# Kernel tuning notes

Hardware: AMD Instinct MI355X
Metric: run time of the kernel (lower is better)

Reference implementation:

```python
import jax, jax.numpy as jnp
import numpy as np

MIMO_RANK = 4  # module constant; q/k are identical across rank and mimo_v=mimo_out=ones,
               # q_bias=k_bias=0, so the rank sum equals MIMO_RANK * single-rank output.


def _rotary(t, ang):
    # split-half rotary: t [..., d], ang [..., d//2]
    d2 = t.shape[-1] // 2
    t1, t2 = t[..., :d2], t[..., d2:]
    c, s = jnp.cos(ang), jnp.sin(ang)
    return jnp.concatenate([t1 * c - t2 * s, t1 * s + t2 * c], axis=-1)


def setup_inputs() -> dict:
    key = jax.random.key(0)
    ks = jax.random.split(key, 6)
    b, l, h, dv, g, dqk = 2, 4096, 32, 64, 1, 128
    x = jax.random.normal(ks[0], (b, l, h, dv), jnp.float32)
    # positive step sizes (discretization dt)
    dt = jax.random.uniform(ks[1], (b, l, h), jnp.float32) * 0.05 + 1e-3
    # negative decay rates so exp(A*dt) < 1
    A = -(jax.random.uniform(ks[2], (h,), jnp.float32) + 0.5)
    B_gate = jax.random.normal(ks[3], (b, l, g, dqk), jnp.float32)
    C_gate = jax.random.normal(ks[4], (b, l, g, dqk), jnp.float32)
    D = jax.random.normal(ks[5], (h,), jnp.float32)
    return {"x": x, "dt": dt, "A": A, "B_gate": B_gate, "C_gate": C_gate,
            "D": D, "chunk_size": 64}


def reference(x, dt, A, B_gate, C_gate, D, chunk_size):
    # Mamba3 MIMO chunked selective scan (SSD) with rotary QK decay.
    # Recurrence per (b, h):  H_t = exp(A_h*dt_t) * H_{t-1} + rot(k_t) (dt_t x_t)^T
    #                         y_t = rot(q_t)^T H_t * MIMO_RANK + D_h * x_t
    # where q=C_gate, k=B_gate (shared across heads, ngroups=1) and the rotary
    # angle is theta_t = cumsum(dt) (TILELANG_ROTARY_DIV=2 -> dqk//2 angles).
    b, l, h, dv = x.shape
    dqk = C_gate.shape[-1]
    c = chunk_size
    n = l // c

    ang = jnp.cumsum(dt, axis=1)[..., None]                     # [b,l,h,1]
    ang = jnp.broadcast_to(ang, (b, l, h, dqk // 2))
    q = jnp.broadcast_to(C_gate[:, :, 0, :][:, :, None, :], (b, l, h, dqk))
    k = jnp.broadcast_to(B_gate[:, :, 0, :][:, :, None, :], (b, l, h, dqk))
    rotq = _rotary(q, ang)                                      # [b,l,h,dqk]
    rotk = _rotary(k, ang)
    adt = A[None, None, :] * dt                                 # [b,l,h] log-decay

    chunk = lambda t: t.reshape(b, n, c, *t.shape[2:])
    rq, rk = chunk(rotq), chunk(rotk)                           # [b,n,c,h,dqk]
    u = chunk(dt[..., None] * x)                                # [b,n,c,h,dv]
    a = chunk(adt)                                              # [b,n,c,h]
    cum = jnp.cumsum(a, axis=2)                                 # within-chunk cum log-decay

    # ---- intra-chunk (quadratic within chunk) ----
    seg = cum[:, :, :, None, :] - cum[:, :, None, :, :]         # [b,n,t,s,h]
    mask = jnp.tril(jnp.ones((c, c), bool))
    L = jnp.where(mask[None, None, :, :, None], jnp.exp(seg), 0.0)
    S = jnp.einsum('bnthd,bnshd->bntsh', rq, rk)                # [b,n,t,s,h]
    y_intra = jnp.einsum('bntsh,bnshe->bnthe', S * L, u)        # [b,n,c,h,dv]

    # ---- inter-chunk state recurrence ----
    decay_to_end = jnp.exp(cum[:, :, -1:, :] - cum)             # [b,n,c,h]
    dH = jnp.einsum('bnshd,bnsh,bnshe->bnhde', rk, decay_to_end, u)  # [b,n,h,dqk,dv]
    cdecay = jnp.exp(cum[:, :, -1, :])                          # [b,n,h] full-chunk decay

    def step(H, inp):
        dc, dh = inp
        Hprev = H
        return dc[:, :, None, None] * H + dh, Hprev

    H0 = jnp.zeros((b, h, dqk, dv), x.dtype)
    _, Hprev = jax.lax.scan(step, H0,
                            (jnp.moveaxis(cdecay, 1, 0), jnp.moveaxis(dH, 1, 0)))
    Hprev = jnp.moveaxis(Hprev, 0, 1)                           # [b,n,h,dqk,dv]

    y_inter = jnp.einsum('bnthd,bnth,bnhde->bnthe', rq, jnp.exp(cum), Hprev)

    y = MIMO_RANK * (y_intra + y_inter).reshape(b, l, h, dv)
    return y + D[None, None, :, None] * x
```

## Files before the change

kernel.cpp:

```cpp
#include <hip/hip_runtime.h>
#include <hip/hip_bf16.h>

#define BB 2
#define LL 4096
#define HH 32
#define DV 64
#define DQK 128
#define CC 64
#define NN 64
#define MIMO_RANK 4.0f

typedef __attribute__((ext_vector_type(8))) short short8;
typedef __attribute__((ext_vector_type(4))) float f32x4;

__device__ __forceinline__ ushort f2bf(float f) {
    uint u = __float_as_uint(f);
    u += 0x7FFF + ((u >> 16) & 1);
    return (ushort)(u >> 16);
}
__device__ __forceinline__ float bfbits2f(uint lo16) {
    return __uint_as_float(lo16 << 16);
}
__device__ __forceinline__ uint pkbf2(float lo, float hi) {
    return (uint)f2bf(lo) | ((uint)f2bf(hi) << 16);
}
union U8 { uint u[4]; short8 s; };

__device__ __forceinline__ int rk_off(int s, int d) {
    return s * 128 + (((((d >> 3) & 15) ^ (s & 7)) << 3)) + (d & 7);
}
__device__ __forceinline__ int rkT_off(int d, int s) {
    return d * 64 + ((((s >> 3) ^ (d & 7)) & 7) << 3) + (s & 7);
}
__device__ __forceinline__ int uwT_off(int e, int s) {
    return e * 64 + ((((s >> 3) ^ (e & 7)) & 7) << 3) + (s & 7);
}
__device__ __forceinline__ int fSL(int t) {
    return (((t & 3) << 1) ^ ((t >> 2) & 7)) & 7;
}
__device__ __forceinline__ int SL_off(int t, int s) {
    return t * 64 + ((((s >> 3) ^ fSL(t)) & 7) << 3) + (s & 7);
}

__device__ __forceinline__ void make_rot_frags(const float* __restrict__ G,
                                               size_t gb, float cv, float sv,
                                               int kgrp, short8* fr) {
    #pragma unroll
    for (int kk = 0; kk < 4; ++kk) {
        int d0 = kk * 32 + kgrp;
        int dl = d0 & 63;
        bool low = d0 < 64;
        float4 a1 = *(const float4*)(G + gb + dl);
        float4 b1 = *(const float4*)(G + gb + dl + 4);
        float4 a2 = *(const float4*)(G + gb + dl + 64);
        float4 b2 = *(const float4*)(G + gb + dl + 68);
        float v0, v1, v2, v3, v4, v5, v6, v7;
        if (low) {
            v0 = a1.x * cv - a2.x * sv; v1 = a1.y * cv - a2.y * sv;
            v2 = a1.z * cv - a2.z * sv; v3 = a1.w * cv - a2.w * sv;
            v4 = b1.x * cv - b2.x * sv; v5 = b1.y * cv - b2.y * sv;
            v6 = b1.z * cv - b2.z * sv; v7 = b1.w * cv - b2.w * sv;
        } else {
            v0 = a1.x * sv + a2.x * cv; v1 = a1.y * sv + a2.y * cv;
            v2 = a1.z * sv + a2.z * cv; v3 = a1.w * sv + a2.w * cv;
            v4 = b1.x * sv + b2.x * cv; v5 = b1.y * sv + b2.y * cv;
            v6 = b1.z * sv + b2.z * cv; v7 = b1.w * sv + b2.w * cv;
        }
        U8 r;
        r.u[0] = pkbf2(v0, v1); r.u[1] = pkbf2(v2, v3);
        r.u[2] = pkbf2(v4, v5); r.u[3] = pkbf2(v6, v7);
        fr[kk] = r.s;
    }
}

__global__ __launch_bounds__(256) void k_scan_dt(const float* __restrict__ dt,
                                                 float* __restrict__ ang) {
    int bh = blockIdx.x;
    int b = bh / HH, h = bh % HH;
    int tid = threadIdx.x;
    const int PT = LL / 256;
    float v[PT];
    float s = 0.f;
    int tbase = tid * PT;
    for (int i = 0; i < PT; ++i) {
        v[i] = dt[(((size_t)b * LL + tbase + i) * HH) + h];
        s += v[i];
    }
    int lane = tid & 63, wv = tid >> 6;
    float ps = s;
    for (int off = 1; off < 64; off <<= 1) {
        float o = __shfl_up(ps, off, 64);
        if (lane >= off) ps += o;
    }
    __shared__ float wsum[4];
    if (lane == 63) wsum[wv] = ps;
    __syncthreads();
    float wadd = 0.f;
    for (int w = 0; w < wv; ++w) wadd += wsum[w];
    float run = wadd + ps - s;
    for (int i = 0; i < PT; ++i) {
        run += v[i];
        ang[(((size_t)b * LL + tbase + i) * HH) + h] = run;
    }
}

__global__ __launch_bounds__(256, 3) void k_intra(
    const float* __restrict__ x, const float* __restrict__ dt,
    const float* __restrict__ A, const float* __restrict__ Bg,
    const float* __restrict__ Cg, const float* __restrict__ ang,
    const float* __restrict__ Dd,
    float* __restrict__ out, ushort* __restrict__ dH,
    float* __restrict__ cdecay) {
    int n = blockIdx.x, h = blockIdx.y, b = blockIdx.z;
    int tid = threadIdx.x;
    int t0 = n * CC;

    __shared__ ushort rkS[CC * DQK];
    __shared__ ushort rkT[DQK * CC];
    __shared__ ushort uwT[DV * CC];
    __shared__ ushort SLs[CC * CC];
    __shared__ float angs[CC], csv[CC], ssv[CC], dw2[CC];

    float Ah = A[h];

    float my_dt = 0.f;
    if (tid < CC) {
        float a = ang[(((size_t)b * LL + t0 + tid) * HH) + h];
        angs[tid] = a;
        float sv, cv;
        __sincosf(a, &sv, &cv);
        csv[tid] = cv;
        ssv[tid] = sv;
        my_dt = dt[(((size_t)b * LL + t0 + tid) * HH) + h];
    }
    __syncthreads();
    float aend = angs[CC - 1];
    if (tid < CC) {
        dw2[tid] = my_dt * __expf(Ah * (aend - angs[tid]));
    }
    if (tid == 0) {
        float angPrev = (t0 == 0) ? 0.f
                                  : ang[(((size_t)b * LL + t0 - 1) * HH) + h];
        cdecay[(b * NN + n) * HH + h] = __expf(Ah * (aend - angPrev));
    }

    #pragma unroll
    for (int it = 0; it < 2; ++it) {
        int w = tid + 256 * it;
        int s = w >> 3, oct = w & 7;
        size_t gb = ((size_t)b * LL + t0 + s) * DQK;
        const float* p = Bg + gb + 8 * oct;
        float4 a0 = *(const float4*)(p);
        float4 a1 = *(const float4*)(p + 4);
        float4 b0 = *(const float4*)(p + 64);
        float4 b1 = *(const float4*)(p + 68);
        float cv = csv[s], sv = ssv[s];
        U8 lo, hi;
        lo.u[0] = pkbf2(a0.x * cv - b0.x * sv, a0.y * cv - b0.y * sv);
        lo.u[1] = pkbf2(a0.z * cv - b0.z * sv, a0.w * cv - b0.w * sv);
        lo.u[2] = pkbf2(a1.x * cv - b1.x * sv, a1.y * cv - b1.y * sv);
        lo.u[3] = pkbf2(a1.z * cv - b1.z * sv, a1.w * cv - b1.w * sv);
        hi.u[0] = pkbf2(a0.x * sv + b0.x * cv, a0.y * sv + b0.y * cv);
        hi.u[1] = pkbf2(a0.z * sv + b0.z * cv, a0.w * sv + b0.w * cv);
        hi.u[2] = pkbf2(a1.x * sv + b1.x * cv, a1.y * sv + b1.y * cv);
        hi.u[3] = pkbf2(a1.z * sv + b1.z * cv, a1.w * sv + b1.w * cv);
        *(short8*)&rkS[rk_off(s, 8 * oct)] = lo.s;
        *(short8*)&rkS[rk_off(s, 8 * oct + 64)] = hi.s;
    }

    int wv = tid >> 6, lane = tid & 63;
    int lrow = lane & 15;
    int g = lane >> 4;
    int kgrp = g * 8;
    int orow = g * 4;

    int t_own = 16 * wv + lrow;
    short8 aq[4];
    make_rot_frags(Cg, ((size_t)b * LL + t0 + t_own) * DQK,
                   csv[t_own], ssv[t_own], kgrp, aq);

    __syncthreads();

    #pragma unroll
    for (int it = 0; it < 2; ++it) {
        int w = tid + 256 * it;
        int e = w & 63, soct = w >> 6;
        int s0 = 8 * soct;
        U8 pk;
        #pragma unroll
        for (int jp = 0; jp < 4; ++jp) {
            int s_a = s0 + 2 * jp, s_b = s_a + 1;
            float xa = x[((((size_t)b * LL + t0 + s_a) * HH) + h) * DV + e] * dw2[s_a];
            float xb = x[((((size_t)b * LL + t0 + s_b) * HH) + h) * DV + e] * dw2[s_b];
            pk.u[jp] = pkbf2(xa, xb);
        }
        *(short8*)&uwT[uwT_off(e, s0)] = pk.s;
    }
    #pragma unroll
    for (int it = 0; it < 4; ++it) {
        int w = tid + 256 * it;
        int d = w & 127, soct = w >> 7;
        int s0 = 8 * soct;
        uint v[8];
        #pragma unroll
        for (int j = 0; j < 8; ++j) v[j] = rkS[rk_off(s0 + j, d)];
        U8 pk;
        pk.u[0] = v[0] | (v[1] << 16);
        pk.u[1] = v[2] | (v[3] << 16);
        pk.u[2] = v[4] | (v[5] << 16);
        pk.u[3] = v[6] | (v[7] << 16);
        *(short8*)&rkT[rkT_off(d, s0)] = pk.s;
    }

    f32x4 accS[4] = {{0.f,0.f,0.f,0.f},{0.f,0.f,0.f,0.f},
                     {0.f,0.f,0.f,0.f},{0.f,0.f,0.f,0.f}};
    #pragma unroll
    for (int kk = 0; kk < 4; ++kk) {
        #pragma unroll
        for (int nt = 0; nt < 4; ++nt) {
            int s = 16 * nt + lrow;
            const short8 bfr = *(const short8*)&rkS[rk_off(s, 32 * kk + kgrp)];
            accS[nt] = __builtin_amdgcn_mfma_f32_16x16x32_bf16(
                aq[kk], bfr, accS[nt], 0, 0, 0);
        }
    }
    #pragma unroll
    for (int rr = 0; rr < 4; ++rr) {
        int t = 16 * wv + orow + rr;
        float etv = __expf(Ah * (angs[t] - aend));
        #pragma unroll
        for (int nt = 0; nt < 4; ++nt) {
            int s = 16 * nt + lrow;
            float v = (t >= s) ? accS[nt][rr] * etv : 0.f;
            SLs[SL_off(t, s)] = f2bf(v);
        }
    }
    __syncthreads();

    {
        f32x4 accY[4] = {{0.f,0.f,0.f,0.f},{0.f,0.f,0.f,0.f},
                         {0.f,0.f,0.f,0.f},{0.f,0.f,0.f,0.f}};
        #pragma unroll
        for (int kk = 0; kk < 2; ++kk) {
            const short8 a = *(const short8*)&SLs[SL_off(16 * wv + lrow, 32 * kk + kgrp)];
            #pragma unroll
            for (int nt = 0; nt < 4; ++nt) {
                const short8 bfr = *(const short8*)&uwT[uwT_off(16 * nt + lrow, 32 * kk + kgrp)];
                accY[nt] = __builtin_amdgcn_mfma_f32_16x16x32_bf16(
                    a, bfr, accY[nt], 0, 0, 0);
            }
        }
        float Dh = Dd[h];
        #pragma unroll
        for (int nt = 0; nt < 4; ++nt) {
            int e = 16 * nt + lrow;
            #pragma unroll
            for (int rr = 0; rr < 4; ++rr) {
                int t = 16 * wv + orow + rr;
                size_t oidx = ((((size_t)b * LL + t0 + t) * HH) + h) * DV + e;
                out[oidx] = MIMO_RANK * accY[nt][rr] + Dh * x[oidx];
            }
        }
    }

    {
        f32x4 accH[2][4] = {{{0.f,0.f,0.f,0.f},{0.f,0.f,0.f,0.f},
                             {0.f,0.f,0.f,0.f},{0.f,0.f,0.f,0.f}},
                            {{0.f,0.f,0.f,0.f},{0.f,0.f,0.f,0.f},
                             {0.f,0.f,0.f,0.f},{0.f,0.f,0.f,0.f}}};
        #pragma unroll
        for (int kk = 0; kk < 2; ++kk) {
            #pragma unroll
            for (int mt = 0; mt < 2; ++mt) {
                const short8 a = *(const short8*)&rkT[rkT_off(32 * wv + 16 * mt + lrow, 32 * kk + kgrp)];
                #pragma unroll
                for (int nt = 0; nt < 4; ++nt) {
                    const short8 bfr = *(const short8*)&uwT[uwT_off(16 * nt + lrow, 32 * kk + kgrp)];
                    accH[mt][nt] = __builtin_amdgcn_mfma_f32_16x16x32_bf16(
                        a, bfr, accH[mt][nt], 0, 0, 0);
                }
            }
        }
        ushort* dHp = dH + (((size_t)(b * NN + n) * HH) + h) * (DQK * DV);
        #pragma unroll
        for (int q = 0; q < 4; ++q) {
            int mt = q >> 1, np = q & 1;
            U8 st;
            st.u[0] = pkbf2(accH[mt][2 * np][0], accH[mt][2 * np][1]);
            st.u[1] = pkbf2(accH[mt][2 * np][2], accH[mt][2 * np][3]);
            st.u[2] = pkbf2(accH[mt][2 * np + 1][0], accH[mt][2 * np + 1][1]);
            st.u[3] = pkbf2(accH[mt][2 * np + 1][2], accH[mt][2 * np + 1][3]);
            *(short8*)(dHp + ((size_t)(wv * 4 + q) * 64 + lane) * 8) = st.s;
        }
    }
}

__global__ __launch_bounds__(256) void k_scan_chunks(
    uint* __restrict__ dH, const float* __restrict__ cdecay) {
    uint f = blockIdx.x * 256 + threadIdx.x;
    int b = (int)(f >> 17);
    uint r = f & 0x1FFFF;
    int h = (int)((r >> 12) & 31);
    uint base = ((uint)b << 23) | r;
    const float* cd = cdecay + (size_t)b * NN * HH + h;
    float h0 = 0.f, h1 = 0.f;
    for (int n = 0; n < NN; ++n) {
        uint a = base + ((uint)n << 17);
        uint v = dH[a];
        float v0 = bfbits2f(v & 0xFFFF), v1 = bfbits2f(v >> 16);
        dH[a] = pkbf2(h0, h1);
        float c = cd[n * HH];
        h0 = c * h0 + v0;
        h1 = c * h1 + v1;
    }
}

__global__ __launch_bounds__(256, 4) void k_inter(
    const float* __restrict__ A, const float* __restrict__ Cg,
    const float* __restrict__ ang, const ushort* __restrict__ Hprev,
    float* __restrict__ out) {
    int n = blockIdx.x, h = blockIdx.y, b = blockIdx.z;
    int tid = threadIdx.x;
    int t0 = n * CC;

    __shared__ __align__(16) uint Hp[16 * 260];
    __shared__ float csv[CC], ssv[CC], gs[CC], angs[CC];
    __shared__ float angPrev_s;

    float Ah = A[h];
    if (tid < CC) {
        float a = ang[(((size_t)b * LL + t0 + tid) * HH) + h];
        angs[tid] = a;
        float sv, cv;
        __sincosf(a, &sv, &cv);
        csv[tid] = cv;
        ssv[tid] = sv;
    }
    if (tid == 0)
        angPrev_s = (t0 == 0) ? 0.f : ang[(((size_t)b * LL + t0 - 1) * HH) + h];
    __syncthreads();
    if (tid < CC) gs[tid] = __expf(Ah * (angs[tid] - angPrev_s));

    const uint* Hsrc = (const uint*)(Hprev + (((size_t)(b * NN + n) * HH) + h) * (DQK * DV));
    #pragma unroll
    for (int it = 0; it < 4; ++it) {
        int p = tid + 256 * it;
        uint4 v = *(const uint4*)(Hsrc + (size_t)p * 4);
        int row = p >> 6, c = p & 63;
        uint4* Hrow = (uint4*)&Hp[row * 260];
        Hrow[c] = v;
    }

    int wv = tid >> 6, lane = tid & 63;
    int lrow = lane & 15;
    int g2 = lane >> 4;
    int kgrp = g2 * 8;
    int orow = g2 * 4;

    int t_own = 16 * wv + lrow;
    short8 aq[4];
    make_rot_frags(Cg, ((size_t)b * LL + t0 + t_own) * DQK,
                   csv[t_own], ssv[t_own], kgrp, aq);
    __syncthreads();

    f32x4 accI[4] = {{0.f,0.f,0.f,0.f},{0.f,0.f,0.f,0.f},
                     {0.f,0.f,0.f,0.f},{0.f,0.f,0.f,0.f}};
    int mt = g2 >> 1;
    int gp0 = 2 * (g2 & 1);
    #pragma unroll
    for (int kk = 0; kk < 4; ++kk) {
        #pragma unroll
        for (int nt = 0; nt < 4; ++nt) {
            int q = mt * 2 + (nt >> 1);
            int row = kk * 4 + q;
            int sb = (nt & 1) * 2;
            const uint2 u0 = *(const uint2*)&Hp[row * 260 + (16 * gp0 + lrow) * 4 + sb];
            const uint2 u1 = *(const uint2*)&Hp[row * 260 + (16 * (gp0 + 1) + lrow) * 4 + sb];
            U8 fr;
            fr.u[0] = u0.x; fr.u[1] = u0.y; fr.u[2] = u1.x; fr.u[3] = u1.y;
            accI[nt] = __builtin_amdgcn_mfma_f32_16x16x32_bf16(
                aq[kk], fr.s, accI[nt], 0, 0, 0);
        }
    }

    #pragma unroll
    for (int rr = 0; rr < 4; ++rr) {
        int t = 16 * wv + orow + rr;
        float g4 = MIMO_RANK * gs[t];
        #pragma unroll
        for (int nt = 0; nt < 4; ++nt) {
            int e = 16 * nt + lrow;
            size_t oidx = ((((size_t)b * LL + t0 + t) * HH) + h) * DV + e;
            out[oidx] += g4 * accI[nt][rr];
        }
    }
}

extern "C" void kernel_launch(void* const* d_in, const int* in_sizes, int n_in,
                              void* d_out, int out_size, void* d_ws,
                              size_t ws_size, hipStream_t stream) {
    (void)in_sizes; (void)n_in; (void)out_size; (void)ws_size;
    const float* x  = (const float*)d_in[0];
    const float* dt = (const float*)d_in[1];
    const float* A  = (const float*)d_in[2];
    const float* Bg = (const float*)d_in[3];
    const float* Cg = (const float*)d_in[4];
    const float* Dd = (const float*)d_in[5];
    float* out = (float*)d_out;
    float* ws  = (float*)d_ws;

    float*  ang    = ws;
    float*  cdecay = ws + 262144;
    ushort* dH     = (ushort*)(ws + 266240);

    k_scan_dt<<<BB * HH, 256, 0, stream>>>(dt, ang);
    k_intra<<<dim3(NN, HH, BB), 256, 0, stream>>>(x, dt, A, Bg, Cg, ang, Dd,
                                                  out, dH, cdecay);
    k_scan_chunks<<<(BB * HH * DQK * DV / 2) / 256, 256, 0, stream>>>(
        (uint*)dH, cdecay);
    k_inter<<<dim3(NN, HH, BB), 256, 0, stream>>>(A, Cg, ang, dH, out);
}
```

Measured before the change: 113.6 us.

## Cut k_intra LDS footprint to raise occupancy by aliasing SL onto rkS

Removes the per-chunk shared arrays for angles, cos/sin and decay weights. Each thread now recomputes these directly from global ang/dt, with redundant sincos and exp calls. The SL tile reuses the rkS buffer after an extra barrier, and launch bounds rise from 3 to 4 blocks per SM. The aim is to shrink LDS so more workgroups fit per CU, at the cost of repeated global loads, duplicated transcendental math, one extra sync and tighter register limits.

```diff
diff --git a/kernel.cpp b/kernel.cpp
--- a/kernel.cpp
+++ b/kernel.cpp
@@ -104,7 +104,7 @@
     }
 }
 
-__global__ __launch_bounds__(256, 3) void k_intra(
+__global__ __launch_bounds__(256, 4) void k_intra(
     const float* __restrict__ x, const float* __restrict__ dt,
     const float* __restrict__ A, const float* __restrict__ Bg,
     const float* __restrict__ Cg, const float* __restrict__ ang,
@@ -118,43 +118,36 @@
     __shared__ ushort rkS[CC * DQK];
     __shared__ ushort rkT[DQK * CC];
     __shared__ ushort uwT[DV * CC];
-    __shared__ ushort SLs[CC * CC];
-    __shared__ float angs[CC], csv[CC], ssv[CC], dw2[CC];
+
+    int wv = tid >> 6, lane = tid & 63;
+    int lrow = lane & 15;
+    int g = lane >> 4;
+    int kgrp = g * 8;
+    int orow = g * 4;
 
     float Ah = A[h];
-
-    float my_dt = 0.f;
-    if (tid < CC) {
-        float a = ang[(((size_t)b * LL + t0 + tid) * HH) + h];
-        angs[tid] = a;
-        float sv, cv;
-        __sincosf(a, &sv, &cv);
-        csv[tid] = cv;
-        ssv[tid] = sv;
-        my_dt = dt[(((size_t)b * LL + t0 + tid) * HH) + h];
-    }
-    __syncthreads();
-    float aend = angs[CC - 1];
-    if (tid < CC) {
-        dw2[tid] = my_dt * __expf(Ah * (aend - angs[tid]));
-    }
+    size_t angBase = ((size_t)b * LL + t0) * HH + h;
+    float aend = ang[angBase + 63 * HH];
+
     if (tid == 0) {
-        float angPrev = (t0 == 0) ? 0.f
-                                  : ang[(((size_t)b * LL + t0 - 1) * HH) + h];
+        float angPrev = (t0 == 0) ? 0.f : ang[angBase - HH];
         cdecay[(b * NN + n) * HH + h] = __expf(Ah * (aend - angPrev));
     }
+
+    const float* BgRow = Bg + ((size_t)b * LL + t0) * DQK;
 
     #pragma unroll
     for (int it = 0; it < 2; ++it) {
         int w = tid + 256 * it;
         int s = w >> 3, oct = w & 7;
-        size_t gb = ((size_t)b * LL + t0 + s) * DQK;
-        const float* p = Bg + gb + 8 * oct;
+        float a = ang[angBase + (size_t)s * HH];
+        float sv, cv;
+        __sincosf(a, &sv, &cv);
+        const float* p = BgRow + s * DQK + 8 * oct;
         float4 a0 = *(const float4*)(p);
         float4 a1 = *(const float4*)(p + 4);
         float4 b0 = *(const float4*)(p + 64);
         float4 b1 = *(const float4*)(p + 68);
-        float cv = csv[s], sv = ssv[s];
         U8 lo, hi;
         lo.u[0] = pkbf2(a0.x * cv - b0.x * sv, a0.y * cv - b0.y * sv);
         lo.u[1] = pkbf2(a0.z * cv - b0.z * sv, a0.w * cv - b0.w * sv);
@@ -168,34 +161,35 @@
         *(short8*)&rkS[rk_off(s, 8 * oct + 64)] = hi.s;
     }
 
-    int wv = tid >> 6, lane = tid & 63;
-    int lrow = lane & 15;
-    int g = lane >> 4;
-    int kgrp = g * 8;
-    int orow = g * 4;
-
-    int t_own = 16 * wv + lrow;
-    short8 aq[4];
-    make_rot_frags(Cg, ((size_t)b * LL + t0 + t_own) * DQK,
-                   csv[t_own], ssv[t_own], kgrp, aq);
-
-    __syncthreads();
-
     #pragma unroll
     for (int it = 0; it < 2; ++it) {
         int w = tid + 256 * it;
-        int e = w & 63, soct = w >> 6;
-        int s0 = 8 * soct;
+        int e = w & 63;
+        int s0 = 8 * (w >> 6);
         U8 pk;
         #pragma unroll
         for (int jp = 0; jp < 4; ++jp) {
             int s_a = s0 + 2 * jp, s_b = s_a + 1;
-            float xa = x[((((size_t)b * LL + t0 + s_a) * HH) + h) * DV + e] * dw2[s_a];
-            float xb = x[((((size_t)b * LL + t0 + s_b) * HH) + h) * DV + e] * dw2[s_b];
+            float dwA = dt[(((size_t)b * LL + t0 + s_a) * HH) + h] *
+                        __expf(Ah * (aend - ang[angBase + (size_t)s_a * HH]));
+            float dwB = dt[(((size_t)b * LL + t0 + s_b) * HH) + h] *
+                        __expf(Ah * (aend - ang[angBase + (size_t)s_b * HH]));
+            float xa = x[((((size_t)b * LL + t0 + s_a) * HH) + h) * DV + e] * dwA;
+            float xb = x[((((size_t)b * LL + t0 + s_b) * HH) + h) * DV + e] * dwB;
             pk.u[jp] = pkbf2(xa, xb);
         }
         *(short8*)&uwT[uwT_off(e, s0)] = pk.s;
     }
+
+    int t_own = 16 * wv + lrow;
+    float a_town = ang[angBase + (size_t)t_own * HH];
+    float cvq, svq;
+    __sincosf(a_town, &svq, &cvq);
+    short8 aq[4];
+    make_rot_frags(Cg, ((size_t)b * LL + t0 + t_own) * DQK, cvq, svq, kgrp, aq);
+
+    __syncthreads();
+
     #pragma unroll
     for (int it = 0; it < 4; ++it) {
         int w = tid + 256 * it;
@@ -224,10 +218,14 @@
                 aq[kk], bfr, accS[nt], 0, 0, 0);
         }
     }
+
+    __syncthreads();
+
+    ushort* SLs = rkS;
     #pragma unroll
     for (int rr = 0; rr < 4; ++rr) {
         int t = 16 * wv + orow + rr;
-        float etv = __expf(Ah * (angs[t] - aend));
+        float etv = __expf(Ah * (ang[angBase + (size_t)t * HH] - aend));
         #pragma unroll
         for (int nt = 0; nt < 4; ++nt) {
             int s = 16 * nt + lrow;
@@ -235,6 +233,7 @@
             SLs[SL_off(t, s)] = f2bf(v);
         }
     }
+
     __syncthreads();
 
     {
```

After: 116.6 us. 2.6% more time.
